# Kernel tuning notes

Measured on AMD Instinct MI355X. Metric: run time of the kernel, lower is better.

## Reference

```python
import jax, jax.numpy as jnp
import numpy as np

B, S, D = 8, 2048, 768
DK = 768
OUT = 10
EPS = 1e-5

def _layernorm(x, w, b):
    mu = jnp.mean(x, axis=-1, keepdims=True)
    var = jnp.mean(jnp.square(x - mu), axis=-1, keepdims=True)
    return (x - mu) * jax.lax.rsqrt(var + EPS) * w + b

def setup_inputs() -> dict:
    key = jax.random.key(0)
    ks = jax.random.split(key, 8)
    sc_in = 1.0 / np.sqrt(D)
    sc_k = 1.0 / np.sqrt(DK)
    return {
        "src": jax.random.normal(ks[0], (B, S, D), dtype=jnp.float32),
        # weights stored as [in, out] so y = x @ W (equivalent to torch x @ W.T)
        "Wq": jax.random.uniform(ks[1], (D, DK), jnp.float32, -sc_in, sc_in),
        "Wk": jax.random.uniform(ks[2], (D, DK), jnp.float32, -sc_in, sc_in),
        "Wv": jax.random.uniform(ks[3], (D, DK), jnp.float32, -sc_in, sc_in),
        "Wo": jax.random.uniform(ks[4], (DK, D), jnp.float32, -sc_k, sc_k),
        "bo": jnp.zeros((D,), jnp.float32),
        "ln1_w": jnp.ones((D,), jnp.float32),
        "ln1_b": jnp.zeros((D,), jnp.float32),
        "ln2_w": jnp.ones((D,), jnp.float32),
        "ln2_b": jnp.zeros((D,), jnp.float32),
        "Wc": jax.random.uniform(ks[5], (D, OUT), jnp.float32, -sc_in, sc_in),
        "bc": jnp.zeros((OUT,), jnp.float32),
    }

def reference(src, Wq, Wk, Wv, Wo, bo, ln1_w, ln1_b, ln2_w, ln2_b, Wc, bc):
    # Attention (dropout in eval mode -> identity)
    Q = src @ Wq  # [B,S,DK]
    K = src @ Wk
    V = src @ Wv
    scores = jnp.einsum('bsd,btd->bst', Q, K) * (DK ** -0.5)
    attn = jax.nn.softmax(scores, axis=-1)
    out = jnp.einsum('bst,btd->bsd', attn, V) @ Wo + bo
    x = src + out
    x = _layernorm(x, ln1_w, ln1_b)
    x = _layernorm(x, ln2_w, ln2_b)
    pooled = jnp.mean(x, axis=1)  # [B,D]
    logits = pooled @ Wc + bc     # [B,OUT]
    return (logits, x)
```

## Files before the change

kernel.cpp:

```cpp
#include <hip/hip_runtime.h>
#include <cmath>

typedef unsigned short ushort_t;
typedef __bf16 bf16x8 __attribute__((ext_vector_type(8)));
typedef float  f32x4  __attribute__((ext_vector_type(4)));

#define B_  8
#define S_  2048
#define D_  768
#define MROWS (B_ * S_)
#define EPS 1e-5f
#define LDST 40

__device__ __forceinline__ float b2f(ushort_t u) {
    union { unsigned int i; float f; } v; v.i = ((unsigned int)u) << 16; return v.f;
}
__device__ __forceinline__ ushort_t f2b(float f) {
    union { float f; unsigned int i; } v; v.f = f;
    unsigned int r = v.i + 0x7fffu + ((v.i >> 16) & 1u);
    return (ushort_t)(r >> 16);
}

__device__ __forceinline__ void gload16(const ushort_t* g, ushort_t* l) {
    __builtin_amdgcn_global_load_lds((__attribute__((address_space(1))) void*)g,
                                     (__attribute__((address_space(3))) void*)l,
                                     16, 0, 0);
}

__global__ void cast_f32_bf16(const float* __restrict__ in, ushort_t* __restrict__ outp, long n)
{
    const long i = ((long)blockIdx.x * 256 + threadIdx.x) * 4;
    if (i + 3 < n) {
        const float4 v = *(const float4*)(in + i);
        ushort4 o;
        o.x = f2b(v.x); o.y = f2b(v.y); o.z = f2b(v.z); o.w = f2b(v.w);
        *(ushort4*)(outp + i) = o;
    }
}

template<int F32IN>
__global__ void transpose_any(const void* __restrict__ srcv, ushort_t* __restrict__ dst,
                              int R, int C, long sb, long db)
{
    __shared__ ushort_t tile[64 * 65];
    dst += (long)blockIdx.z * db;
    const int r0 = blockIdx.y * 64, c0 = blockIdx.x * 64;
    const int t = threadIdx.x;
    const int tr = t >> 6, tc = t & 63;
    #pragma unroll
    for (int i = 0; i < 16; i++) {
        const int r = i * 4 + tr;
        ushort_t v;
        if (F32IN) v = f2b(((const float*)srcv + (long)blockIdx.z * sb)[(long)(r0 + r) * C + (c0 + tc)]);
        else       v = ((const ushort_t*)srcv + (long)blockIdx.z * sb)[(long)(r0 + r) * C + (c0 + tc)];
        tile[r * 65 + tc] = v;
    }
    __syncthreads();
    #pragma unroll
    for (int i = 0; i < 16; i++) {
        const int r = i * 4 + tr;
        dst[(long)(c0 + r) * R + (r0 + tc)] = tile[tc * 65 + r];
    }
}

template<int MODE>
__global__ __launch_bounds__(256)
void gemm_nt(const ushort_t* __restrict__ A, const ushort_t* __restrict__ Bt,
             void* __restrict__ Cv, int M, int N, int Kd,
             long batchA, long batchB, long batchC, float scale,
             const float* __restrict__ bias, const float* __restrict__ resid,
             float* __restrict__ rowsum)
{
    __shared__ __align__(16) ushort_t As[128 * 32];
    __shared__ __align__(16) ushort_t Bs[128 * 32];

    const int bz = blockIdx.z;
    A  += (long)bz * batchA;
    Bt += (long)bz * batchB;

    const int nxt  = gridDim.x;
    const int nblk = nxt * gridDim.y;
    int lin = blockIdx.y * nxt + blockIdx.x;
    if ((nblk & 7) == 0) {
        const int per = nblk >> 3;
        lin = (lin & 7) * per + (lin >> 3);
    }
    const int tile_n = (lin % nxt) * 128;
    const int tile_m = (lin / nxt) * 128;

    const int tid  = threadIdx.x;
    const int w    = tid >> 6;
    const int lane = tid & 63;
    const int wr = w >> 1, wc = w & 1;
    const int r16 = lane & 15;
    const int kq  = lane >> 4;

    const int srow   = lane >> 2;
    const int schunk = lane & 3;
    const int arow0 = w * 32 + srow;
    const int arow1 = arow0 + 16;
    const int g0 = (schunk ^ ((arow0 >> 1) & 3)) * 8;
    const int g1 = (schunk ^ ((arow1 >> 1) & 3)) * 8;

    const ushort_t* Ar0 = A  + (long)(tile_m + arow0) * Kd + g0;
    const ushort_t* Ar1 = A  + (long)(tile_m + arow1) * Kd + g1;
    const ushort_t* Br0 = Bt + (long)(tile_n + arow0) * Kd + g0;
    const ushort_t* Br1 = Bt + (long)(tile_n + arow1) * Kd + g1;

    ushort_t* lA0 = &As[(w * 32     ) * 32];
    ushort_t* lA1 = &As[(w * 32 + 16) * 32];
    ushort_t* lB0 = &Bs[(w * 32     ) * 32];
    ushort_t* lB1 = &Bs[(w * 32 + 16) * 32];

    f32x4 acc[4][4] = {};

    for (int k0 = 0; k0 < Kd; k0 += 32) {
        gload16(Ar0 + k0, lA0);
        gload16(Ar1 + k0, lA1);
        gload16(Br0 + k0, lB0);
        gload16(Br1 + k0, lB1);
        __syncthreads();

        bf16x8 af[4], bg[4];
        #pragma unroll
        for (int i = 0; i < 4; i++) {
            const int ra = wr * 64 + i * 16 + r16;
            af[i] = *reinterpret_cast<const bf16x8*>(&As[ra * 32 + ((kq ^ ((ra >> 1) & 3)) * 8)]);
            const int rb = wc * 64 + i * 16 + r16;
            bg[i] = *reinterpret_cast<const bf16x8*>(&Bs[rb * 32 + ((kq ^ ((rb >> 1) & 3)) * 8)]);
        }
        #pragma unroll
        for (int mi = 0; mi < 4; mi++)
            #pragma unroll
            for (int ni = 0; ni < 4; ni++)
                acc[mi][ni] = __builtin_amdgcn_mfma_f32_16x16x32_bf16(af[mi], bg[ni], acc[mi][ni], 0, 0, 0);
        __syncthreads();
    }

    if (MODE == 0) {
        ushort_t* C = (ushort_t*)Cv + (long)bz * batchC;
        #pragma unroll
        for (int mi = 0; mi < 4; mi++)
            #pragma unroll
            for (int ni = 0; ni < 4; ni++)
                #pragma unroll
                for (int r = 0; r < 4; r++) {
                    const int row = tile_m + wr * 64 + mi * 16 + kq * 4 + r;
                    const int col = tile_n + wc * 64 + ni * 16 + r16;
                    C[(long)row * N + col] = f2b(acc[mi][ni][r] * scale);
                }
    } else if (MODE == 1) {
        float* C = (float*)Cv;
        #pragma unroll
        for (int mi = 0; mi < 4; mi++)
            #pragma unroll
            for (int ni = 0; ni < 4; ni++)
                #pragma unroll
                for (int r = 0; r < 4; r++) {
                    const int row = tile_m + wr * 64 + mi * 16 + kq * 4 + r;
                    const int col = tile_n + wc * 64 + ni * 16 + r16;
                    C[(long)row * N + col] =
                        acc[mi][ni][r] + bias[col] + resid[(long)row * N + col];
                }
    } else if (MODE == 2) {
        ushort_t* C = (ushort_t*)Cv + (long)bz * batchC;
        const float* rs = rowsum + (long)bz * 2048;
        #pragma unroll
        for (int mi = 0; mi < 4; mi++) {
            float inv[4];
            #pragma unroll
            for (int r = 0; r < 4; r++)
                inv[r] = 1.0f / rs[tile_m + wr * 64 + mi * 16 + kq * 4 + r];
            #pragma unroll
            for (int ni = 0; ni < 4; ni++)
                #pragma unroll
                for (int r = 0; r < 4; r++) {
                    const int row = tile_m + wr * 64 + mi * 16 + kq * 4 + r;
                    const int col = tile_n + wc * 64 + ni * 16 + r16;
                    C[(long)row * N + col] = f2b(acc[mi][ni][r] * inv[r]);
                }
        }
    } else if (MODE == 3) {
        ushort_t* C = (ushort_t*)Cv + (long)bz * batchC;
        float* rs = rowsum + (long)bz * 2048;
        #pragma unroll
        for (int mi = 0; mi < 4; mi++)
            #pragma unroll
            for (int r = 0; r < 4; r++) {
                const int row = tile_m + wr * 64 + mi * 16 + kq * 4 + r;
                float psum = 0.f;
                #pragma unroll
                for (int ni = 0; ni < 4; ni++) {
                    const float e = __expf(acc[mi][ni][r] * scale);
                    psum += e;
                    const int col = tile_n + wc * 64 + ni * 16 + r16;
                    C[(long)row * N + col] = f2b(e);
                }
                psum += __shfl_xor(psum, 1);
                psum += __shfl_xor(psum, 2);
                psum += __shfl_xor(psum, 4);
                psum += __shfl_xor(psum, 8);
                if (r16 == 0) atomicAdd(&rs[row], psum);
            }
    } else {
        const int sect  = tile_n / 768;
        const int ncol0 = tile_n - sect * 768;
        ushort_t* C = (ushort_t*)Cv + (size_t)sect * ((size_t)MROWS * 768);
        const float sc = (sect == 0) ? scale : 1.0f;
        #pragma unroll
        for (int mi = 0; mi < 4; mi++)
            #pragma unroll
            for (int ni = 0; ni < 4; ni++)
                #pragma unroll
                for (int r = 0; r < 4; r++) {
                    const int row = tile_m + wr * 64 + mi * 16 + kq * 4 + r;
                    const int col = ncol0 + wc * 64 + ni * 16 + r16;
                    C[(long)row * 768 + col] = f2b(acc[mi][ni][r] * sc);
                }
    }
}

template<int TRANSB, int MODE, int BF32>
__global__ __launch_bounds__(256)
void gemm_s(const ushort_t* __restrict__ A, const void* __restrict__ Bsrc,
            void* __restrict__ Cv, int M, int N, int Kd, float scale,
            const float* __restrict__ bias, const float* __restrict__ resid)
{
    __shared__ __align__(16) ushort_t As[128 * LDST];
    __shared__ __align__(16) ushort_t Bs[128 * LDST];
    const int tile_n = blockIdx.x * 128;
    const int tile_m = blockIdx.y * 128;
    const int tid  = threadIdx.x;
    const int w    = tid >> 6;
    const int lane = tid & 63;
    const int wr = w >> 1, wc = w & 1;
    const int r16 = lane & 15;
    const int kq  = lane >> 4;
    f32x4 acc[4][4] = {};
    for (int k0 = 0; k0 < Kd; k0 += 32) {
        #pragma unroll
        for (int cc = 0; cc < 2; cc++) {
            const int c = tid + cc * 256;
            const int row = c >> 2, col = (c & 3) * 8;
            *(uint4*)&As[row * LDST + col] = *(const uint4*)(A + (long)(tile_m + row) * Kd + k0 + col);
        }
        if (TRANSB == 0) {
            const ushort_t* Bt = (const ushort_t*)Bsrc;
            #pragma unroll
            for (int cc = 0; cc < 2; cc++) {
                const int c = tid + cc * 256;
                const int row = c >> 2, col = (c & 3) * 8;
                *(uint4*)&Bs[row * LDST + col] = *(const uint4*)(Bt + (long)(tile_n + row) * Kd + k0 + col);
            }
        } else {
            #pragma unroll
            for (int i = 0; i < 16; i++) {
                const int lin = i * 256 + tid;
                const int kr = lin >> 7, nc = lin & 127;
                ushort_t bv;
                if (BF32) bv = f2b(((const float*)Bsrc)[(long)(k0 + kr) * N + tile_n + nc]);
                else      bv = ((const ushort_t*)Bsrc)[(long)(k0 + kr) * N + tile_n + nc];
                Bs[nc * LDST + kr] = bv;
            }
        }
        __syncthreads();
        bf16x8 af[4], bg[4];
        #pragma unroll
        for (int i = 0; i < 4; i++) {
            af[i] = *reinterpret_cast<const bf16x8*>(&As[(wr * 64 + i * 16 + r16) * LDST + kq * 8]);
            bg[i] = *reinterpret_cast<const bf16x8*>(&Bs[(wc * 64 + i * 16 + r16) * LDST + kq * 8]);
        }
        #pragma unroll
        for (int mi = 0; mi < 4; mi++)
            #pragma unroll
            for (int ni = 0; ni < 4; ni++)
                acc[mi][ni] = __builtin_amdgcn_mfma_f32_16x16x32_bf16(af[mi], bg[ni], acc[mi][ni], 0, 0, 0);
        __syncthreads();
    }
    if (MODE == 0) {
        ushort_t* C = (ushort_t*)Cv;
        #pragma unroll
        for (int mi = 0; mi < 4; mi++)
            #pragma unroll
            for (int ni = 0; ni < 4; ni++)
                #pragma unroll
                for (int r = 0; r < 4; r++) {
                    const int row = tile_m + wr * 64 + mi * 16 + kq * 4 + r;
                    const int col = tile_n + wc * 64 + ni * 16 + r16;
                    C[(long)row * N + col] = f2b(acc[mi][ni][r] * scale);
                }
    } else {
        float* C = (float*)Cv;
        #pragma unroll
        for (int mi = 0; mi < 4; mi++)
            #pragma unroll
            for (int ni = 0; ni < 4; ni++)
                #pragma unroll
                for (int r = 0; r < 4; r++) {
                    const int row = tile_m + wr * 64 + mi * 16 + kq * 4 + r;
                    const int col = tile_n + wc * 64 + ni * 16 + r16;
                    C[(long)row * N + col] =
                        acc[mi][ni][r] + bias[col] + resid[(long)row * N + col];
                }
    }
}

__global__ void softmax_rows(ushort_t* __restrict__ p)
{
    __shared__ float sm[4], ss_[4];
    ushort_t* pr = p + (long)blockIdx.x * 2048;
    const int tid = threadIdx.x;
    const int w = tid >> 6;
    const uint4 raw = *(const uint4*)(pr + tid * 8);
    float v[8];
    v[0] = b2f((ushort_t)(raw.x & 0xffff)); v[1] = b2f((ushort_t)(raw.x >> 16));
    v[2] = b2f((ushort_t)(raw.y & 0xffff)); v[3] = b2f((ushort_t)(raw.y >> 16));
    v[4] = b2f((ushort_t)(raw.z & 0xffff)); v[5] = b2f((ushort_t)(raw.z >> 16));
    v[6] = b2f((ushort_t)(raw.w & 0xffff)); v[7] = b2f((ushort_t)(raw.w >> 16));
    float mx = -3.0e38f;
    #pragma unroll
    for (int i = 0; i < 8; i++) mx = fmaxf(mx, v[i]);
    #pragma unroll
    for (int off = 32; off; off >>= 1) mx = fmaxf(mx, __shfl_xor(mx, off));
    if ((tid & 63) == 0) sm[w] = mx;
    __syncthreads();
    mx = fmaxf(fmaxf(sm[0], sm[1]), fmaxf(sm[2], sm[3]));
    float s = 0.f;
    #pragma unroll
    for (int i = 0; i < 8; i++) { v[i] = __expf(v[i] - mx); s += v[i]; }
    #pragma unroll
    for (int off = 32; off; off >>= 1) s += __shfl_xor(s, off);
    if ((tid & 63) == 0) ss_[w] = s;
    __syncthreads();
    s = ss_[0] + ss_[1] + ss_[2] + ss_[3];
    const float inv = 1.f / s;
    uint4 o;
    o.x = f2b(v[0] * inv) | ((unsigned)f2b(v[1] * inv) << 16);
    o.y = f2b(v[2] * inv) | ((unsigned)f2b(v[3] * inv) << 16);
    o.z = f2b(v[4] * inv) | ((unsigned)f2b(v[5] * inv) << 16);
    o.w = f2b(v[6] * inv) | ((unsigned)f2b(v[7] * inv) << 16);
    *(uint4*)(pr + tid * 8) = o;
}

__global__ void ln_fused(float* __restrict__ x,
                         const float* __restrict__ w1, const float* __restrict__ b1,
                         const float* __restrict__ w2, const float* __restrict__ b2)
{
    __shared__ float r1s[4], r1q[4], r2s[4], r2q[4];
    const long row = blockIdx.x;
    const int tid = threadIdx.x;
    const int w = tid >> 6;
    float* xr = x + row * 768;
    float v[3], s = 0.f, q = 0.f;
    #pragma unroll
    for (int i = 0; i < 3; i++) { const float t = xr[tid + i * 256]; v[i] = t; s += t; q += t * t; }
    #pragma unroll
    for (int off = 32; off; off >>= 1) { s += __shfl_xor(s, off); q += __shfl_xor(q, off); }
    if ((tid & 63) == 0) { r1s[w] = s; r1q[w] = q; }
    __syncthreads();
    s = r1s[0] + r1s[1] + r1s[2] + r1s[3];
    q = r1q[0] + r1q[1] + r1q[2] + r1q[3];
    float mu = s * (1.f / 768.f);
    float ri = rsqrtf(q * (1.f / 768.f) - mu * mu + EPS);
    float y[3];
    s = 0.f; q = 0.f;
    #pragma unroll
    for (int i = 0; i < 3; i++) {
        const int d = tid + i * 256;
        const float t = (v[i] - mu) * ri * w1[d] + b1[d];
        y[i] = t; s += t; q += t * t;
    }
    #pragma unroll
    for (int off = 32; off; off >>= 1) { s += __shfl_xor(s, off); q += __shfl_xor(q, off); }
    if ((tid & 63) == 0) { r2s[w] = s; r2q[w] = q; }
    __syncthreads();
    s = r2s[0] + r2s[1] + r2s[2] + r2s[3];
    q = r2q[0] + r2q[1] + r2q[2] + r2q[3];
    mu = s * (1.f / 768.f);
    ri = rsqrtf(q * (1.f / 768.f) - mu * mu + EPS);
    #pragma unroll
    for (int i = 0; i < 3; i++) {
        const int d = tid + i * 256;
        xr[d] = (y[i] - mu) * ri * w2[d] + b2[d];
    }
}

__global__ void pool_reduce(const float* __restrict__ x, float* __restrict__ pooled)
{
    const int d  = blockIdx.x * 256 + threadIdx.x;
    const int b  = blockIdx.z;
    const int sp = blockIdx.y;
    const float* base = x + ((long)b * 2048 + sp * 128) * 768 + d;
    float s = 0.f;
    #pragma unroll 8
    for (int i = 0; i < 128; i++) s += base[(long)i * 768];
    atomicAdd(&pooled[b * 768 + d], s);
}

__global__ void logits_kernel(const float* __restrict__ pooled, const float* __restrict__ Wc,
                              const float* __restrict__ bc, float* __restrict__ out)
{
    const int b = blockIdx.x / 10, o = blockIdx.x % 10;
    const int lane = threadIdx.x;
    float s = 0.f;
    #pragma unroll
    for (int d = lane; d < 768; d += 64) s += pooled[b * 768 + d] * Wc[d * 10 + o];
    #pragma unroll
    for (int off = 32; off; off >>= 1) s += __shfl_xor(s, off);
    if (lane == 0) out[b * 10 + o] = s * (1.f / 2048.f) + bc[o];
}

extern "C" void kernel_launch(void* const* d_in, const int* in_sizes, int n_in,
                              void* d_out, int out_size, void* d_ws, size_t ws_size,
                              hipStream_t stream)
{
    (void)in_sizes; (void)n_in; (void)out_size;
    const float* src  = (const float*)d_in[0];
    const float* Wq   = (const float*)d_in[1];
    const float* Wk   = (const float*)d_in[2];
    const float* Wv   = (const float*)d_in[3];
    const float* Wo   = (const float*)d_in[4];
    const float* bo   = (const float*)d_in[5];
    const float* ln1w = (const float*)d_in[6];
    const float* ln1b = (const float*)d_in[7];
    const float* ln2w = (const float*)d_in[8];
    const float* ln2b = (const float*)d_in[9];
    const float* Wc   = (const float*)d_in[10];
    const float* bc   = (const float*)d_in[11];
    float* out = (float*)d_out;

    const dim3 blk(256);
    const float qscale = 1.0f / sqrtf(768.0f);
    const long bs = (long)2048 * 768;

    const size_t WT    = (size_t)768 * 768 * 2;
    const size_t BUF   = (size_t)MROWS * 768 * 2;
    const size_t POOLB = 24576;
    const size_t RSB   = (size_t)B_ * 2048 * 4;
    const size_t PROBS8 = (size_t)8 * 2048 * 2048 * 2;
    const size_t needB = 4 * WT + 5 * BUF + POOLB + RSB;
    const size_t needA = needB + PROBS8;

    char* ws = (char*)d_ws;
    size_t off = 0;
    auto alloc = [&](size_t bytes) { void* p = ws + off; off += (bytes + 255) & ~(size_t)255; return p; };

    if (ws_size >= needB) {
        ushort_t* Wtq  = (ushort_t*)alloc(WT);
        ushort_t* Wtk  = (ushort_t*)alloc(WT);
        ushort_t* Wtv  = (ushort_t*)alloc(WT);
        ushort_t* Wto  = (ushort_t*)alloc(WT);
        ushort_t* srcb = (ushort_t*)alloc(BUF);
        ushort_t* Qb   = (ushort_t*)alloc(BUF);
        ushort_t* Kb   = (ushort_t*)alloc(BUF);
        ushort_t* Vb   = (ushort_t*)alloc(BUF);
        ushort_t* Vt   = (ushort_t*)alloc(BUF);
        float*  pooled = (float*)  alloc(POOLB);
        float*  rowsum = (float*)  alloc(RSB);
        const bool batched = (ws_size >= needA);
        ushort_t* probs = batched ? (ushort_t*)alloc(PROBS8) : srcb;
        ushort_t* attn  = Vb;
        float*    xpre  = out + 80;

        cast_f32_bf16<<<MROWS * 768 / 1024, blk, 0, stream>>>(src, srcb, (long)MROWS * 768);
        transpose_any<1><<<dim3(12, 12, 1), blk, 0, stream>>>(Wq, Wtq, 768, 768, 0, 0);
        transpose_any<1><<<dim3(12, 12, 1), blk, 0, stream>>>(Wk, Wtk, 768, 768, 0, 0);
        transpose_any<1><<<dim3(12, 12, 1), blk, 0, stream>>>(Wv, Wtv, 768, 768, 0, 0);
        transpose_any<1><<<dim3(12, 12, 1), blk, 0, stream>>>(Wo, Wto, 768, 768, 0, 0);

        gemm_nt<4><<<dim3(18, 128, 1), blk, 0, stream>>>(srcb, Wtq, Qb, MROWS, 2304, 768,
                                                         0, 0, 0, qscale, nullptr, nullptr, nullptr);

        transpose_any<0><<<dim3(12, 32, B_), blk, 0, stream>>>(Vb, Vt, 2048, 768, bs, bs);
        hipMemsetAsync(rowsum, 0, RSB, stream);

        if (batched) {
            gemm_nt<3><<<dim3(16, 16, B_), blk, 0, stream>>>(Qb, Kb, probs, 2048, 2048, 768,
                                                             bs, bs, (long)2048 * 2048, 1.0f,
                                                             nullptr, nullptr, rowsum);
            gemm_nt<2><<<dim3(6, 16, B_), blk, 0, stream>>>(probs, Vt, attn, 2048, 768, 2048,
                                                            (long)2048 * 2048, bs, bs, 1.0f,
                                                            nullptr, nullptr, rowsum);
        } else {
            for (int bz = 0; bz < B_; bz += 2) {
                gemm_nt<3><<<dim3(16, 16, 2), blk, 0, stream>>>(Qb + bz * bs, Kb + bz * bs, probs,
                                                                2048, 2048, 768, bs, bs, (long)2048 * 2048,
                                                                1.0f, nullptr, nullptr, rowsum + bz * 2048);
                gemm_nt<2><<<dim3(6, 16, 2), blk, 0, stream>>>(probs, Vt + bz * bs, attn + bz * bs,
                                                               2048, 768, 2048,
                                                               (long)2048 * 2048, bs, bs, 1.0f,
                                                               nullptr, nullptr, rowsum + bz * 2048);
            }
        }

        gemm_nt<1><<<dim3(6, 128, 1), blk, 0, stream>>>(attn, Wto, xpre, MROWS, 768, 768,
                                                        0, 0, 0, 1.0f, bo, src, nullptr);
        ln_fused<<<MROWS, blk, 0, stream>>>(xpre, ln1w, ln1b, ln2w, ln2b);
        hipMemsetAsync(pooled, 0, B_ * 768 * 4, stream);
        pool_reduce<<<dim3(3, 16, B_), blk, 0, stream>>>(xpre, pooled);
        logits_kernel<<<80, 64, 0, stream>>>(pooled, Wc, bc, out);
    } else {
        ushort_t* srcb = (ushort_t*)alloc(BUF);
        ushort_t* Qb   = (ushort_t*)alloc(BUF);
        ushort_t* Kb   = (ushort_t*)alloc(BUF);
        ushort_t* Vb   = (ushort_t*)alloc(BUF);
        float*  pooled = (float*)  alloc(POOLB);
        ushort_t* probs = srcb;
        ushort_t* attn  = Qb;
        float*    xpre  = out + 80;

        cast_f32_bf16<<<MROWS * 768 / 1024, blk, 0, stream>>>(src, srcb, (long)MROWS * 768);
        gemm_s<1, 0, 1><<<dim3(6, 128), blk, 0, stream>>>(srcb, Wq, Qb, MROWS, 768, 768, qscale, nullptr, nullptr);
        gemm_s<1, 0, 1><<<dim3(6, 128), blk, 0, stream>>>(srcb, Wk, Kb, MROWS, 768, 768, 1.0f, nullptr, nullptr);
        gemm_s<1, 0, 1><<<dim3(6, 128), blk, 0, stream>>>(srcb, Wv, Vb, MROWS, 768, 768, 1.0f, nullptr, nullptr);
        for (int bz = 0; bz < B_; bz++) {
            gemm_s<0, 0, 0><<<dim3(16, 16), blk, 0, stream>>>(Qb + bz * bs, Kb + bz * bs, probs,
                                                              2048, 2048, 768, 1.0f, nullptr, nullptr);
            softmax_rows<<<2048, blk, 0, stream>>>(probs);
            gemm_s<1, 0, 0><<<dim3(6, 16), blk, 0, stream>>>(probs, Vb + bz * bs, attn + bz * bs,
                                                             2048, 768, 2048, 1.0f, nullptr, nullptr);
        }
        gemm_s<1, 1, 1><<<dim3(6, 128), blk, 0, stream>>>(attn, Wo, xpre, MROWS, 768, 768, 1.0f, bo, src);
        ln_fused<<<MROWS, blk, 0, stream>>>(xpre, ln1w, ln1b, ln2w, ln2b);
        hipMemsetAsync(pooled, 0, B_ * 768 * 4, stream);
        pool_reduce<<<dim3(3, 16, B_), blk, 0, stream>>>(xpre, pooled);
        logits_kernel<<<80, 64, 0, stream>>>(pooled, Wc, bc, out);
    }
}
```

Before: 474.1 us.

## Add 256x256-tile 512-thread GEMM kernel with pipelined LDS staging for all GEMMs

Introduces a new GEMM kernel with 256x256 output tiles, 8 waves per block and a 64-wide K step. It streams A and B into double-buffered, XOR-swizzled LDS in quarter chunks interleaved with MFMA phases, and remaps blocks in a grouped order for L2 locality. All four GEMMs in the batched path (QKV, scores+exp, PV, output projection) now use it, which should raise arithmetic intensity and overlap global loads with compute. The trade-offs are heavy LDS use (128KB) and register pressure, fewer blocks (e.g. 192 for the projection GEMMs), and many barriers per K step.

```diff
diff --git a/kernel.cpp b/kernel.cpp
--- a/kernel.cpp
+++ b/kernel.cpp
@@ -60,6 +60,232 @@
     for (int i = 0; i < 16; i++) {
         const int r = i * 4 + tr;
         dst[(long)(c0 + r) * R + (r0 + tc)] = tile[tc * 65 + r];
+    }
+}
+
+
+__device__ __forceinline__ void stage_half256(const ushort_t* __restrict__ g, int row0,
+                                              int Kd, int k0, ushort_t* l, int tid)
+{
+    #pragma unroll
+    for (int i = 0; i < 2; i++) {
+        const int c   = i * 512 + tid;
+        const int row = c >> 3;
+        const int scol = ((c & 7) ^ (((row >> 2) & 1) << 1)) * 8;
+        gload16(g + (long)(row0 + row) * Kd + (k0 + scol), l + c * 8);
+    }
+}
+
+#define G256_BAR() do { \
+    asm volatile("" ::: "memory"); \
+    __builtin_amdgcn_s_barrier(); \
+    asm volatile("" ::: "memory"); \
+} while (0)
+
+#define G256_LGKM0() asm volatile("s_waitcnt lgkmcnt(0)" ::: "memory")
+
+#define G256_READ_A(q) do { \
+    _Pragma("unroll") \
+    for (int m2 = 0; m2 < 2; m2++) { \
+        _Pragma("unroll") \
+        for (int s = 0; s < 2; s++) { \
+            int lb = (((q) * 2 + m2) * 16 + r16) * 128 + s * 64 + kq * 16; \
+            lb ^= ((lb >> 9) & 1) << 5; \
+            af[m2][s] = *reinterpret_cast<const bf16x8*>(LAc + (lb >> 1)); \
+        } \
+    } \
+} while (0)
+
+#define G256_MFMA(q) do { \
+    __builtin_amdgcn_s_setprio(1); \
+    _Pragma("unroll") \
+    for (int m2 = 0; m2 < 2; m2++) { \
+        _Pragma("unroll") \
+        for (int ni = 0; ni < 4; ni++) { \
+            acc[(q) * 2 + m2][ni] = __builtin_amdgcn_mfma_f32_16x16x32_bf16(af[m2][0], bg[ni][0], acc[(q) * 2 + m2][ni], 0, 0, 0); \
+            acc[(q) * 2 + m2][ni] = __builtin_amdgcn_mfma_f32_16x16x32_bf16(af[m2][1], bg[ni][1], acc[(q) * 2 + m2][ni], 0, 0, 0); \
+        } \
+    } \
+    __builtin_amdgcn_s_setprio(0); \
+} while (0)
+
+template<int MODE>
+__global__ __launch_bounds__(512, 2)
+void gemm256(const ushort_t* __restrict__ A, const ushort_t* __restrict__ Bt,
+             void* __restrict__ Cv, int M, int N, int Kd,
+             long batchA, long batchB, long batchC, float scale,
+             const float* __restrict__ bias, const float* __restrict__ resid,
+             float* __restrict__ rowsum)
+{
+    __shared__ __align__(16) ushort_t lds[65536];
+
+    const int bz = blockIdx.z;
+    A  += (long)bz * batchA;
+    Bt += (long)bz * batchB;
+
+    const int nxt  = gridDim.x;
+    const int nblk = nxt * gridDim.y;
+    int lin = blockIdx.y * nxt + blockIdx.x;
+    if ((nblk & 7) == 0) {
+        const int per = nblk >> 3;
+        lin = (lin & 7) * per + (lin >> 3);
+    }
+    const int tile_n = (lin % nxt) * 256;
+    const int tile_m = (lin / nxt) * 256;
+
+    const int tid  = threadIdx.x;
+    const int w    = tid >> 6;
+    const int lane = tid & 63;
+    const int wr   = w >> 2;
+    const int wc   = w & 3;
+    const int r16  = lane & 15;
+    const int kq   = lane >> 4;
+    const int brow = (wc & 1) * 64;
+
+    const int NT = Kd >> 6;
+
+    ushort_t* const sA = lds;
+    ushort_t* const sB = lds + 16384;
+    const ushort_t* const LA0 = lds + wr * 8192;
+    const ushort_t* const LB0 = lds + 16384 + (wc >> 1) * 8192;
+
+    f32x4 acc[8][4] = {};
+
+    stage_half256(A,  tile_m,       Kd, 0,  sA,         tid);
+    stage_half256(A,  tile_m + 128, Kd, 0,  sA + 8192,  tid);
+    stage_half256(Bt, tile_n,       Kd, 0,  sB,         tid);
+    stage_half256(Bt, tile_n + 128, Kd, 0,  sB + 8192,  tid);
+    if (NT > 1) {
+        stage_half256(Bt, tile_n,       Kd, 64, sB + 32768,        tid);
+        stage_half256(Bt, tile_n + 128, Kd, 64, sB + 32768 + 8192, tid);
+        asm volatile("s_waitcnt vmcnt(4)" ::: "memory");
+    } else {
+        asm volatile("s_waitcnt vmcnt(0)" ::: "memory");
+    }
+    G256_BAR();
+
+    int cur = 0;
+    for (int t = 0; t < NT; ++t) {
+        const int k0 = t << 6;
+        const ushort_t* LAc = LA0 + cur * 32768;
+        const ushort_t* LBc = LB0 + cur * 32768;
+        ushort_t* const nA  = sA + (cur ^ 1) * 32768;
+        ushort_t* const nB  = sB + cur * 32768;
+
+        bf16x8 bg[4][2], af[2][2];
+
+        #pragma unroll
+        for (int ni = 0; ni < 4; ni++)
+            #pragma unroll
+            for (int s = 0; s < 2; s++) {
+                int lb = (brow + ni * 16 + r16) * 128 + s * 64 + kq * 16;
+                lb ^= ((lb >> 9) & 1) << 5;
+                bg[ni][s] = *reinterpret_cast<const bf16x8*>(LBc + (lb >> 1));
+            }
+        G256_READ_A(0);
+        if (t + 1 < NT) stage_half256(A, tile_m, Kd, k0 + 64, nA, tid);
+        G256_BAR();
+        G256_LGKM0();
+        G256_MFMA(0);
+        G256_LGKM0();
+        G256_BAR();
+
+        G256_READ_A(1);
+        if (t + 1 < NT) stage_half256(A, tile_m + 128, Kd, k0 + 64, nA + 8192, tid);
+        G256_BAR();
+        G256_LGKM0();
+        G256_MFMA(1);
+        G256_LGKM0();
+        G256_BAR();
+
+        G256_READ_A(2);
+        if (t + 2 < NT) stage_half256(Bt, tile_n, Kd, k0 + 128, nB, tid);
+        G256_BAR();
+        G256_LGKM0();
+        G256_MFMA(2);
+        G256_LGKM0();
+        G256_BAR();
+
+        G256_READ_A(3);
+        if (t + 2 < NT) stage_half256(Bt, tile_n + 128, Kd, k0 + 128, nB + 8192, tid);
+        G256_BAR();
+        G256_LGKM0();
+        G256_MFMA(3);
+        G256_LGKM0();
+        if (t + 2 < NT) { asm volatile("s_waitcnt vmcnt(4)" ::: "memory"); }
+        else            { asm volatile("s_waitcnt vmcnt(0)" ::: "memory"); }
+        G256_BAR();
+        cur ^= 1;
+    }
+
+    if (MODE == 1) {
+        float* C = (float*)Cv;
+        #pragma unroll
+        for (int mi = 0; mi < 8; mi++)
+            #pragma unroll
+            for (int ni = 0; ni < 4; ni++)
+                #pragma unroll
+                for (int r = 0; r < 4; r++) {
+                    const int row = tile_m + wr * 128 + mi * 16 + kq * 4 + r;
+                    const int col = tile_n + wc * 64 + ni * 16 + r16;
+                    C[(long)row * N + col] =
+                        acc[mi][ni][r] + bias[col] + resid[(long)row * N + col];
+                }
+    } else if (MODE == 2) {
+        ushort_t* C = (ushort_t*)Cv + (long)bz * batchC;
+        const float* rs = rowsum + (long)bz * 2048;
+        #pragma unroll
+        for (int mi = 0; mi < 8; mi++) {
+            float inv[4];
+            #pragma unroll
+            for (int r = 0; r < 4; r++)
+                inv[r] = 1.0f / rs[tile_m + wr * 128 + mi * 16 + kq * 4 + r];
+            #pragma unroll
+            for (int ni = 0; ni < 4; ni++)
+                #pragma unroll
+                for (int r = 0; r < 4; r++) {
+                    const int row = tile_m + wr * 128 + mi * 16 + kq * 4 + r;
+                    const int col = tile_n + wc * 64 + ni * 16 + r16;
+                    C[(long)row * N + col] = f2b(acc[mi][ni][r] * inv[r]);
+                }
+        }
+    } else if (MODE == 3) {
+        ushort_t* C = (ushort_t*)Cv + (long)bz * batchC;
+        float* rs = rowsum + (long)bz * 2048;
+        #pragma unroll
+        for (int mi = 0; mi < 8; mi++)
+            #pragma unroll
+            for (int r = 0; r < 4; r++) {
+                const int row = tile_m + wr * 128 + mi * 16 + kq * 4 + r;
+                float psum = 0.f;
+                #pragma unroll
+                for (int ni = 0; ni < 4; ni++) {
+                    const float e = __expf(acc[mi][ni][r] * scale);
+                    psum += e;
+                    const int col = tile_n + wc * 64 + ni * 16 + r16;
+                    C[(long)row * N + col] = f2b(e);
+                }
+                psum += __shfl_xor(psum, 1);
+                psum += __shfl_xor(psum, 2);
+                psum += __shfl_xor(psum, 4);
+                psum += __shfl_xor(psum, 8);
+                if (r16 == 0) atomicAdd(&rs[row], psum);
+            }
+    } else {
+        const int sect  = tile_n / 768;
+        const int ncol0 = tile_n - sect * 768;
+        ushort_t* C = (ushort_t*)Cv + (size_t)sect * ((size_t)MROWS * 768);
+        const float sc = (sect == 0) ? scale : 1.0f;
+        #pragma unroll
+        for (int mi = 0; mi < 8; mi++)
+            #pragma unroll
+            for (int ni = 0; ni < 4; ni++)
+                #pragma unroll
+                for (int r = 0; r < 4; r++) {
+                    const int row = tile_m + wr * 128 + mi * 16 + kq * 4 + r;
+                    const int col = ncol0 + wc * 64 + ni * 16 + r16;
+                    C[(long)row * 768 + col] = f2b(acc[mi][ni][r] * sc);
+                }
     }
 }
 
@@ -430,6 +656,7 @@
     float* out = (float*)d_out;
 
     const dim3 blk(256);
+    const dim3 blk512(512);
     const float qscale = 1.0f / sqrtf(768.0f);
     const long bs = (long)2048 * 768;
 
@@ -468,19 +695,19 @@
         transpose_any<1><<<dim3(12, 12, 1), blk, 0, stream>>>(Wv, Wtv, 768, 768, 0, 0);
         transpose_any<1><<<dim3(12, 12, 1), blk, 0, stream>>>(Wo, Wto, 768, 768, 0, 0);
 
-        gemm_nt<4><<<dim3(18, 128, 1), blk, 0, stream>>>(srcb, Wtq, Qb, MROWS, 2304, 768,
-                                                         0, 0, 0, qscale, nullptr, nullptr, nullptr);
+        gemm256<4><<<dim3(9, 64, 1), blk512, 0, stream>>>(srcb, Wtq, Qb, MROWS, 2304, 768,
+                                                          0, 0, 0, qscale, nullptr, nullptr, nullptr);
 
         transpose_any<0><<<dim3(12, 32, B_), blk, 0, stream>>>(Vb, Vt, 2048, 768, bs, bs);
         hipMemsetAsync(rowsum, 0, RSB, stream);
 
         if (batched) {
-            gemm_nt<3><<<dim3(16, 16, B_), blk, 0, stream>>>(Qb, Kb, probs, 2048, 2048, 768,
-                                                             bs, bs, (long)2048 * 2048, 1.0f,
-                                                             nullptr, nullptr, rowsum);
-            gemm_nt<2><<<dim3(6, 16, B_), blk, 0, stream>>>(probs, Vt, attn, 2048, 768, 2048,
-                                                            (long)2048 * 2048, bs, bs, 1.0f,
-                                                            nullptr, nullptr, rowsum);
+            gemm256<3><<<dim3(8, 8, B_), blk512, 0, stream>>>(Qb, Kb, probs, 2048, 2048, 768,
+                                                              bs, bs, (long)2048 * 2048, 1.0f,
+                                                              nullptr, nullptr, rowsum);
+            gemm256<2><<<dim3(3, 8, B_), blk512, 0, stream>>>(probs, Vt, attn, 2048, 768, 2048,
+                                                              (long)2048 * 2048, bs, bs, 1.0f,
+                                                              nullptr, nullptr, rowsum);
         } else {
             for (int bz = 0; bz < B_; bz += 2) {
                 gemm_nt<3><<<dim3(16, 16, 2), blk, 0, stream>>>(Qb + bz * bs, Kb + bz * bs, probs,
@@ -493,8 +720,8 @@
             }
         }
 
-        gemm_nt<1><<<dim3(6, 128, 1), blk, 0, stream>>>(attn, Wto, xpre, MROWS, 768, 768,
-                                                        0, 0, 0, 1.0f, bo, src, nullptr);
+        gemm256<1><<<dim3(3, 64, 1), blk512, 0, stream>>>(attn, Wto, xpre, MROWS, 768, 768,
+                                                          0, 0, 0, 1.0f, bo, src, nullptr);
         ln_fused<<<MROWS, blk, 0, stream>>>(xpre, ln1w, ln1b, ln2w, ln2b);
         hipMemsetAsync(pooled, 0, B_ * 768 * 4, stream);
         pool_reduce<<<dim3(3, 16, B_), blk, 0, stream>>>(xpre, pooled);
```

After: 455.3 us. 1.04x faster.
